# Optimization experiments

Hardware: AMD Instinct MI355X
Metric: run time of the kernel (lower is better)

## Reference

```python
import jax, jax.numpy as jnp
import numpy as np
from jax import lax

IN_CHANNELS = 64
PYRAMID_LEVELS = 3
SIGMA = 1.6
S_VALUE = 2.0 ** (1.0 / 3.0)


def _gaussian_kernel_2d(ksize, sigma):
    # matches cv2.getGaussianKernel: normalized 1D gaussian, then outer product
    ax = np.arange(ksize, dtype=np.float64) - (ksize - 1) / 2.0
    g = np.exp(-(ax ** 2) / (2.0 * sigma ** 2))
    g = g / g.sum()
    return np.outer(g, g).astype(np.float32)


def _depthwise_kernels():
    # list of (C, 1, k, k) depthwise kernels, k = 3, 5, 7
    ks = []
    for i in range(PYRAMID_LEVELS):
        k2d = _gaussian_kernel_2d(2 * i + 3, SIGMA * (S_VALUE ** i))
        w = np.broadcast_to(k2d[None, None], (IN_CHANNELS, 1) + k2d.shape)
        ks.append(jnp.asarray(np.ascontiguousarray(w)))
    return ks


def setup_inputs() -> dict:
    key = jax.random.key(0)
    x = jax.random.normal(key, (16, IN_CHANNELS, 256, 256), dtype=jnp.float32)
    return {"x": x}


def reference(x):
    B, C, H, W = x.shape
    kernels = _depthwise_kernels()
    G = x
    pyramid = [G]
    for w in kernels:
        G = lax.conv_general_dilated(
            G, w, window_strides=(1, 1), padding="SAME",
            feature_group_count=C,
            dimension_numbers=("NCHW", "OIHW", "NCHW"))
        pyramid.append(G)
    # Laplacian levels and their sum
    L0 = pyramid[0] - pyramid[1]
    L1 = pyramid[1] - pyramid[2]
    L2 = pyramid[2] - pyramid[3]
    context = (L0 + L1 + L2).reshape(B, C, H * W)  # (B, d, HW)
    att = jnp.einsum("bdn,ben->bde", jax.nn.softmax(context, axis=2), context)
    return att
```

## Files before the change

### kernel.cpp

```cpp
#include <hip/hip_runtime.h>
#include <hip/hip_bf16.h>
#include <math.h>

typedef short bf16x8 __attribute__((ext_vector_type(8)));
typedef float f32x4  __attribute__((ext_vector_type(4)));

struct WC   { float c[13]; };
struct G157 { float g3[3], g5[5], g7[7]; };

__device__ __forceinline__ unsigned short f2bf(float f) {
  __hip_bfloat16 h = __float2bfloat16(f);
  return *reinterpret_cast<unsigned short*>(&h);
}

__global__ __launch_bounds__(256) void zero_k(float* __restrict__ out, float* __restrict__ S,
                                              float* __restrict__ wtab, G157 gw) {
  int i = blockIdx.x * 256 + threadIdx.x;
  if (i < 65536) out[i] = 0.f;
  if (i < 1024) S[i] = 0.f;
  if (blockIdx.x == 0) {
    int g = threadIdx.x;
    float row[13];
    #pragma unroll
    for (int t = 0; t < 13; ++t) row[t] = 0.f;
    #pragma unroll
    for (int di = -3; di <= 3; ++di) {
      int ii = g + di;
      if ((unsigned)ii >= 256u) continue;
      float w7 = gw.g7[di + 3];
      #pragma unroll
      for (int dj = -2; dj <= 2; ++dj) {
        int jj = ii + dj;
        if ((unsigned)jj >= 256u) continue;
        float c2 = w7 * gw.g5[dj + 2];
        #pragma unroll
        for (int dk = -1; dk <= 1; ++dk) {
          int mm = jj + dk;
          if ((unsigned)mm >= 256u) continue;
          row[di + dj + dk + 6] += c2 * gw.g3[dk + 1];
        }
      }
    }
    #pragma unroll
    for (int t = 0; t < 13; ++t) wtab[(g << 4) + t] = row[t];
    wtab[(g << 4) + 13] = 0.f; wtab[(g << 4) + 14] = 0.f; wtab[(g << 4) + 15] = 0.f;
  }
}

__global__ __launch_bounds__(256) void ctx_k(const float* __restrict__ x,
                                             unsigned short* __restrict__ ctxb,
                                             const float* __restrict__ wtab,
                                             WC wc) {
  __shared__ __align__(16) float rb[2][8][272];
  __shared__ float vs[64][24];
  __shared__ float wl[96];

  const int tid = threadIdx.x;
  const int img = blockIdx.x >> 2;
  const int band = blockIdx.x & 3;
  const int y0 = band << 6;
  const float* xg = x + ((size_t)img << 16);
  unsigned short* cgb = ctxb + ((size_t)img << 16);

  if (tid < 96) wl[tid] = wtab[tid];
  {
    int bb = tid >> 7, rr = (tid >> 4) & 7, pp = tid & 15;
    rb[bb][rr][(pp < 8) ? pp : (256 + pp)] = 0.f;
  }

  float win[32];
  #pragma unroll
  for (int i = 0; i < 32; ++i) win[i] = 0.f;
  #pragma unroll
  for (int i = 0; i < 20; ++i) {
    int yy = y0 - 6 + i;
    if ((unsigned)yy < 256u) win[i] = xg[yy * 256 + tid];
  }
  __syncthreads();

  const bool vsave = (tid < 12) || (tid >= 244);
  const int vsidx = (tid < 12) ? tid : (tid - 232);
  const int g = tid >> 6, q = tid & 63;

  #pragma unroll
  for (int it = 0; it < 8; ++it) {
    const int y = y0 + 8 * it;
    #pragma unroll
    for (int j = 0; j < 8; ++j) {
      if (8 * it + 14 + j < 70) {
        int yy = y + 14 + j;
        float v = 0.f;
        if (yy < 256) v = xg[yy * 256 + tid];
        win[(8 * it + 20 + j) & 31] = v;
      }
    }
    float vv[8];
    const bool topb = (band == 0 && it == 0), botb = (band == 3 && it == 7);
    if (!topb && !botb) {
      #pragma unroll
      for (int r = 0; r < 8; ++r) {
        float a = 0.f;
        #pragma unroll
        for (int t = 0; t < 13; ++t) a += wc.c[t] * win[(8 * it + r + t) & 31];
        vv[r] = a;
      }
    } else {
      #pragma unroll
      for (int r = 0; r < 8; ++r) {
        int yr = y + r;
        float a = 0.f;
        if (yr < 6) {
          #pragma unroll
          for (int t = 0; t < 13; ++t) a += wl[(yr << 4) + t] * win[(8 * it + r + t) & 31];
        } else if (yr > 249) {
          #pragma unroll
          for (int t = 0; t < 13; ++t) a += wl[((255 - yr) << 4) + (12 - t)] * win[(8 * it + r + t) & 31];
        } else {
          #pragma unroll
          for (int t = 0; t < 13; ++t) a += wc.c[t] * win[(8 * it + r + t) & 31];
        }
        vv[r] = a;
      }
    }
    const int buf = it & 1;
    #pragma unroll
    for (int r = 0; r < 8; ++r) rb[buf][r][8 + tid] = vv[r];
    if (vsave) {
      #pragma unroll
      for (int r = 0; r < 8; ++r) vs[8 * it + r][vsidx] = vv[r];
    }
    __syncthreads();

    #pragma unroll
    for (int u = 0; u < 2; ++u) {
      const int rr = 2 * g + u;
      const int yy = y + rr;
      const float* hp = &rb[buf][rr][4 * q];
      float f[20];
      *(float4*)&f[0]  = *(const float4*)(hp + 0);
      *(float4*)&f[4]  = *(const float4*)(hp + 4);
      *(float4*)&f[8]  = *(const float4*)(hp + 8);
      *(float4*)&f[12] = *(const float4*)(hp + 12);
      *(float4*)&f[16] = *(const float4*)(hp + 16);
      float4 xq = *(const float4*)(xg + yy * 256 + 4 * q);
      float h0 = 0.f, h1 = 0.f, h2 = 0.f, h3 = 0.f;
      #pragma unroll
      for (int t = 0; t < 13; ++t) {
        float w = wc.c[t];
        h0 += w * f[2 + t]; h1 += w * f[3 + t]; h2 += w * f[4 + t]; h3 += w * f[5 + t];
      }
      unsigned short s0 = f2bf(xq.x - h0), s1 = f2bf(xq.y - h1);
      unsigned short s2 = f2bf(xq.z - h2), s3 = f2bf(xq.w - h3);
      *(ushort4*)(cgb + (size_t)yy * 256 + 4 * q) = make_ushort4(s0, s1, s2, s3);
    }
  }

  __syncthreads();
  #pragma unroll
  for (int k = 0; k < 3; ++k) {
    int e = k * 256 + tid;
    int row = e / 12;
    int ce = e - row * 12;
    int col = (ce < 6) ? ce : (244 + ce);
    float h = 0.f;
    if (ce < 6) {
      #pragma unroll
      for (int t = 0; t < 13; ++t) {
        int vc = col - 6 + t;
        if (vc >= 0) h += wl[(col << 4) + t] * vs[row][vc];
      }
    } else {
      #pragma unroll
      for (int t = 0; t < 13; ++t) {
        int vc = col - 6 + t;
        if (vc < 256) h += wl[((255 - col) << 4) + (12 - t)] * vs[row][vc - 232];
      }
    }
    int yrow = y0 + row;
    float xval = xg[yrow * 256 + col];
    cgb[yrow * 256 + col] = f2bf(xval - h);
  }
}

__global__ __launch_bounds__(256) void att_k(const unsigned short* __restrict__ ctxb,
                                             float* __restrict__ S,
                                             float* __restrict__ attacc) {
  const int t = threadIdx.x;
  const int wv = t >> 6, lane = t & 63;
  const int rw = lane & 15;
  const int kq = lane >> 4;
  const int ci = blockIdx.x;
  const int b = blockIdx.y;
  const unsigned short* cb = ctxb + ((size_t)b << 22);
  const int n0 = (ci << 10) + (kq << 3);

  const unsigned short* pA = cb + (((size_t)(16 * wv + rw)) << 16) + n0;
  const unsigned short* pB = cb + (((size_t)rw) << 16) + n0;

  f32x4 acc0 = {0.f, 0.f, 0.f, 0.f}, acc1 = acc0, acc2 = acc0, acc3 = acc0;
  float ssum = 0.f;

  #pragma unroll 8
  for (int ks = 0; ks < 1024; ks += 32) {
    bf16x8 av = *(const bf16x8*)(pA + ks);
    bf16x8 ev;
    const unsigned* au = (const unsigned*)&av;
    unsigned* eu = (unsigned*)&ev;
    #pragma unroll
    for (int j = 0; j < 4; ++j) {
      unsigned w = au[j];
      float elo = __expf(__uint_as_float(w << 16));
      float ehi = __expf(__uint_as_float(w & 0xffff0000u));
      ssum += elo + ehi;
      eu[j] = ((unsigned)f2bf(ehi) << 16) | (unsigned)f2bf(elo);
    }
    bf16x8 b0 = *(const bf16x8*)(pB + ks);
    bf16x8 b1 = *(const bf16x8*)(pB + (size_t)(16 << 16) + ks);
    bf16x8 b2 = *(const bf16x8*)(pB + (size_t)(32 << 16) + ks);
    bf16x8 b3 = *(const bf16x8*)(pB + (size_t)(48 << 16) + ks);
    acc0 = __builtin_amdgcn_mfma_f32_16x16x32_bf16(ev, b0, acc0, 0, 0, 0);
    acc1 = __builtin_amdgcn_mfma_f32_16x16x32_bf16(ev, b1, acc1, 0, 0, 0);
    acc2 = __builtin_amdgcn_mfma_f32_16x16x32_bf16(ev, b2, acc2, 0, 0, 0);
    acc3 = __builtin_amdgcn_mfma_f32_16x16x32_bf16(ev, b3, acc3, 0, 0, 0);
  }

  ssum += __shfl_xor(ssum, 16);
  ssum += __shfl_xor(ssum, 32);
  if (lane < 16) atomicAdd(&S[(b << 6) + (wv << 4) + rw], ssum);

  const int dl = kq << 2;
  float* ap = attacc + (((size_t)((b << 6) + (wv << 4) + dl)) << 6) + rw;
  #pragma unroll
  for (int reg = 0; reg < 4; ++reg) {
    atomicAdd(ap + ((size_t)reg << 6) + 0,  acc0[reg]);
    atomicAdd(ap + ((size_t)reg << 6) + 16, acc1[reg]);
    atomicAdd(ap + ((size_t)reg << 6) + 32, acc2[reg]);
    atomicAdd(ap + ((size_t)reg << 6) + 48, acc3[reg]);
  }
}

__global__ __launch_bounds__(256) void fin_k(float* __restrict__ out, const float* __restrict__ S) {
  int i = blockIdx.x * 256 + threadIdx.x;
  out[i] = out[i] / S[i >> 6];
}

extern "C" void kernel_launch(void* const* d_in, const int* in_sizes, int n_in,
                              void* d_out, int out_size, void* d_ws, size_t ws_size,
                              hipStream_t stream) {
  const float* x = (const float*)d_in[0];
  float* out = (float*)d_out;
  unsigned short* ctxb = (unsigned short*)d_ws;
  float* S    = (float*)((char*)d_ws + (size_t)67108864 * 2);
  float* wtab = (float*)((char*)d_ws + (size_t)67108864 * 2 + 4096);
  if (ws_size < (size_t)67108864 * 2 + 4096 + 16384) return;

  double gg[3][7];
  double sv = pow(2.0, 1.0 / 3.0);
  for (int lv = 0; lv < 3; ++lv) {
    int k = 2 * lv + 3;
    double sig = 1.6 * pow(sv, lv), sum = 0.0;
    for (int i = 0; i < k; ++i) {
      double a = i - (k - 1) / 2.0;
      gg[lv][i] = exp(-a * a / (2.0 * sig * sig));
      sum += gg[lv][i];
    }
    for (int i = 0; i < k; ++i) gg[lv][i] /= sum;
  }

  G157 gw;
  for (int i = 0; i < 3; ++i) gw.g3[i] = (float)gg[0][i];
  for (int i = 0; i < 5; ++i) gw.g5[i] = (float)gg[1][i];
  for (int i = 0; i < 7; ++i) gw.g7[i] = (float)gg[2][i];

  WC wc;
  {
    double t35[7] = {0};
    for (int i = 0; i < 3; ++i)
      for (int j = 0; j < 5; ++j) t35[i + j] += gg[0][i] * gg[1][j];
    double t357[13] = {0};
    for (int i = 0; i < 7; ++i)
      for (int j = 0; j < 7; ++j) t357[i + j] += t35[i] * gg[2][j];
    for (int t = 0; t < 13; ++t) wc.c[t] = (float)t357[t];
  }

  zero_k<<<dim3(256), dim3(256), 0, stream>>>(out, S, wtab, gw);
  ctx_k<<<dim3(4096), dim3(256), 0, stream>>>(x, ctxb, wtab, wc);
  att_k<<<dim3(64, 16), dim3(256), 0, stream>>>(ctxb, S, out);
  fin_k<<<dim3(256), dim3(256), 0, stream>>>(out, S);
}
```

Before: 207.8 us.

## Restructure context kernel into per-wave row strips without block barriers

The separable-blur context kernel now gives each wave its own 16-row strip. Each thread keeps a float4 register ring of input rows, and the horizontal pass goes through a wave-private shared buffer. This removes the per-iteration block-wide __syncthreads and the double-buffered row staging, and it reuses the centre input row from the ring instead of reloading it from global memory. Loads become vectorised float4, and launch bounds ask for three blocks per CU; the trade-off is more register pressure and reliance on in-order LDS access within a wave.

Result: slower. 218.3 us (+5.0%).

```diff
diff --git a/kernel.cpp b/kernel.cpp
--- a/kernel.cpp
+++ b/kernel.cpp
@@ -47,138 +47,140 @@
   }
 }
 
-__global__ __launch_bounds__(256) void ctx_k(const float* __restrict__ x,
-                                             unsigned short* __restrict__ ctxb,
-                                             const float* __restrict__ wtab,
-                                             WC wc) {
-  __shared__ __align__(16) float rb[2][8][272];
-  __shared__ float vs[64][24];
+__global__ __launch_bounds__(256, 3) void ctx_k(const float* __restrict__ x,
+                                                unsigned short* __restrict__ ctxb,
+                                                const float* __restrict__ wtab,
+                                                WC wc) {
+  __shared__ __align__(16) float vb[4][272];
+  __shared__ __align__(16) float evs[4][16][24];
   __shared__ float wl[96];
 
   const int tid = threadIdx.x;
-  const int img = blockIdx.x >> 2;
-  const int band = blockIdx.x & 3;
-  const int y0 = band << 6;
+  const int w = tid >> 6, q = tid & 63;
+  const int img = blockIdx.x >> 2, band = blockIdx.x & 3;
+  const int r0 = (band << 6) + (w << 4);
+  const int c0 = q << 2;
   const float* xg = x + ((size_t)img << 16);
   unsigned short* cgb = ctxb + ((size_t)img << 16);
 
   if (tid < 96) wl[tid] = wtab[tid];
-  {
-    int bb = tid >> 7, rr = (tid >> 4) & 7, pp = tid & 15;
-    rb[bb][rr][(pp < 8) ? pp : (256 + pp)] = 0.f;
-  }
-
-  float win[32];
-  #pragma unroll
-  for (int i = 0; i < 32; ++i) win[i] = 0.f;
-  #pragma unroll
-  for (int i = 0; i < 20; ++i) {
-    int yy = y0 - 6 + i;
-    if ((unsigned)yy < 256u) win[i] = xg[yy * 256 + tid];
+  if (q < 2) {
+    *(float4*)&vb[w][q << 2] = make_float4(0.f, 0.f, 0.f, 0.f);
+    *(float4*)&vb[w][264 + (q << 2)] = make_float4(0.f, 0.f, 0.f, 0.f);
   }
   __syncthreads();
 
-  const bool vsave = (tid < 12) || (tid >= 244);
-  const int vsidx = (tid < 12) ? tid : (tid - 232);
-  const int g = tid >> 6, q = tid & 63;
-
-  #pragma unroll
-  for (int it = 0; it < 8; ++it) {
-    const int y = y0 + 8 * it;
-    #pragma unroll
-    for (int j = 0; j < 8; ++j) {
-      if (8 * it + 14 + j < 70) {
-        int yy = y + 14 + j;
-        float v = 0.f;
-        if (yy < 256) v = xg[yy * 256 + tid];
-        win[(8 * it + 20 + j) & 31] = v;
-      }
-    }
-    float vv[8];
-    const bool topb = (band == 0 && it == 0), botb = (band == 3 && it == 7);
-    if (!topb && !botb) {
-      #pragma unroll
-      for (int r = 0; r < 8; ++r) {
-        float a = 0.f;
-        #pragma unroll
-        for (int t = 0; t < 13; ++t) a += wc.c[t] * win[(8 * it + r + t) & 31];
-        vv[r] = a;
+  float4 ring[16];
+  #pragma unroll
+  for (int i = 0; i < 15; ++i) {
+    int yy = r0 - 6 + i;
+    float4 v = make_float4(0.f, 0.f, 0.f, 0.f);
+    if ((unsigned)yy < 256u) v = *(const float4*)(xg + yy * 256 + c0);
+    ring[i] = v;
+  }
+  ring[15] = make_float4(0.f, 0.f, 0.f, 0.f);
+
+  #pragma unroll
+  for (int rr = 0; rr < 16; ++rr) {
+    {
+      int yy = r0 + rr + 9;
+      float4 v = make_float4(0.f, 0.f, 0.f, 0.f);
+      if (yy < 256) v = *(const float4*)(xg + yy * 256 + c0);
+      ring[(rr + 15) & 15] = v;
+    }
+    const int y = r0 + rr;
+
+    float ax = 0.f, ay = 0.f, az = 0.f, aw = 0.f;
+    if (rr >= 6 && rr <= 9) {
+      #pragma unroll
+      for (int t = 0; t < 13; ++t) {
+        float4 s = ring[(rr + t) & 15];
+        float wv = wc.c[t];
+        ax += wv * s.x; ay += wv * s.y; az += wv * s.z; aw += wv * s.w;
+      }
+    } else if (rr < 6) {
+      if (y >= 6) {
+        #pragma unroll
+        for (int t = 0; t < 13; ++t) {
+          float4 s = ring[(rr + t) & 15];
+          float wv = wc.c[t];
+          ax += wv * s.x; ay += wv * s.y; az += wv * s.z; aw += wv * s.w;
+        }
+      } else {
+        #pragma unroll
+        for (int t = 0; t < 13; ++t) {
+          float4 s = ring[(rr + t) & 15];
+          float wv = wl[(y << 4) + t];
+          ax += wv * s.x; ay += wv * s.y; az += wv * s.z; aw += wv * s.w;
+        }
       }
     } else {
-      #pragma unroll
-      for (int r = 0; r < 8; ++r) {
-        int yr = y + r;
-        float a = 0.f;
-        if (yr < 6) {
-          #pragma unroll
-          for (int t = 0; t < 13; ++t) a += wl[(yr << 4) + t] * win[(8 * it + r + t) & 31];
-        } else if (yr > 249) {
-          #pragma unroll
-          for (int t = 0; t < 13; ++t) a += wl[((255 - yr) << 4) + (12 - t)] * win[(8 * it + r + t) & 31];
-        } else {
-          #pragma unroll
-          for (int t = 0; t < 13; ++t) a += wc.c[t] * win[(8 * it + r + t) & 31];
-        }
-        vv[r] = a;
-      }
-    }
-    const int buf = it & 1;
-    #pragma unroll
-    for (int r = 0; r < 8; ++r) rb[buf][r][8 + tid] = vv[r];
-    if (vsave) {
-      #pragma unroll
-      for (int r = 0; r < 8; ++r) vs[8 * it + r][vsidx] = vv[r];
-    }
-    __syncthreads();
-
-    #pragma unroll
-    for (int u = 0; u < 2; ++u) {
-      const int rr = 2 * g + u;
-      const int yy = y + rr;
-      const float* hp = &rb[buf][rr][4 * q];
-      float f[20];
-      *(float4*)&f[0]  = *(const float4*)(hp + 0);
-      *(float4*)&f[4]  = *(const float4*)(hp + 4);
-      *(float4*)&f[8]  = *(const float4*)(hp + 8);
-      *(float4*)&f[12] = *(const float4*)(hp + 12);
-      *(float4*)&f[16] = *(const float4*)(hp + 16);
-      float4 xq = *(const float4*)(xg + yy * 256 + 4 * q);
-      float h0 = 0.f, h1 = 0.f, h2 = 0.f, h3 = 0.f;
-      #pragma unroll
-      for (int t = 0; t < 13; ++t) {
-        float w = wc.c[t];
-        h0 += w * f[2 + t]; h1 += w * f[3 + t]; h2 += w * f[4 + t]; h3 += w * f[5 + t];
-      }
-      unsigned short s0 = f2bf(xq.x - h0), s1 = f2bf(xq.y - h1);
-      unsigned short s2 = f2bf(xq.z - h2), s3 = f2bf(xq.w - h3);
-      *(ushort4*)(cgb + (size_t)yy * 256 + 4 * q) = make_ushort4(s0, s1, s2, s3);
-    }
-  }
-
-  __syncthreads();
+      if (y <= 249) {
+        #pragma unroll
+        for (int t = 0; t < 13; ++t) {
+          float4 s = ring[(rr + t) & 15];
+          float wv = wc.c[t];
+          ax += wv * s.x; ay += wv * s.y; az += wv * s.z; aw += wv * s.w;
+        }
+      } else {
+        #pragma unroll
+        for (int t = 0; t < 13; ++t) {
+          float4 s = ring[(rr + t) & 15];
+          float wv = wl[((255 - y) << 4) + (12 - t)];
+          ax += wv * s.x; ay += wv * s.y; az += wv * s.z; aw += wv * s.w;
+        }
+      }
+    }
+
+    float4 v4 = make_float4(ax, ay, az, aw);
+    *(float4*)&vb[w][8 + c0] = v4;
+    if (q < 3)       *(float4*)&evs[w][rr][c0] = v4;
+    else if (q >= 61) *(float4*)&evs[w][rr][12 + ((q - 61) << 2)] = v4;
+
+    const float* hp = &vb[w][c0];
+    float f[20];
+    *(float4*)&f[0]  = *(const float4*)(hp + 0);
+    *(float4*)&f[4]  = *(const float4*)(hp + 4);
+    *(float4*)&f[8]  = *(const float4*)(hp + 8);
+    *(float4*)&f[12] = *(const float4*)(hp + 12);
+    *(float4*)&f[16] = *(const float4*)(hp + 16);
+    float h0 = 0.f, h1 = 0.f, h2 = 0.f, h3 = 0.f;
+    #pragma unroll
+    for (int t = 0; t < 13; ++t) {
+      float wv = wc.c[t];
+      h0 += wv * f[2 + t]; h1 += wv * f[3 + t]; h2 += wv * f[4 + t]; h3 += wv * f[5 + t];
+    }
+    float4 xq = ring[(rr + 6) & 15];
+    unsigned short s0 = f2bf(xq.x - h0), s1 = f2bf(xq.y - h1);
+    unsigned short s2 = f2bf(xq.z - h2), s3 = f2bf(xq.w - h3);
+    *(ushort4*)(cgb + (size_t)y * 256 + c0) = make_ushort4(s0, s1, s2, s3);
+  }
+
   #pragma unroll
   for (int k = 0; k < 3; ++k) {
-    int e = k * 256 + tid;
+    int e = (k << 6) + q;
     int row = e / 12;
     int ce = e - row * 12;
+    int y = r0 + row;
     int col = (ce < 6) ? ce : (244 + ce);
     float h = 0.f;
     if (ce < 6) {
       #pragma unroll
       for (int t = 0; t < 13; ++t) {
         int vc = col - 6 + t;
-        if (vc >= 0) h += wl[(col << 4) + t] * vs[row][vc];
+        int vi = (vc < 0) ? 0 : vc;
+        h += wl[(col << 4) + t] * evs[w][row][vi];
       }
     } else {
       #pragma unroll
       for (int t = 0; t < 13; ++t) {
         int vc = col - 6 + t;
-        if (vc < 256) h += wl[((255 - col) << 4) + (12 - t)] * vs[row][vc - 232];
-      }
-    }
-    int yrow = y0 + row;
-    float xval = xg[yrow * 256 + col];
-    cgb[yrow * 256 + col] = f2bf(xval - h);
+        int vi = (vc > 255 ? 255 : vc) - 232;
+        h += wl[((255 - col) << 4) + (12 - t)] * evs[w][row][vi];
+      }
+    }
+    float xv = xg[(size_t)y * 256 + col];
+    cgb[(size_t)y * 256 + col] = f2bf(xv - h);
   }
 }
 
@@ -208,9 +210,9 @@
     unsigned* eu = (unsigned*)&ev;
     #pragma unroll
     for (int j = 0; j < 4; ++j) {
-      unsigned w = au[j];
-      float elo = __expf(__uint_as_float(w << 16));
-      float ehi = __expf(__uint_as_float(w & 0xffff0000u));
+      unsigned ww = au[j];
+      float elo = __expf(__uint_as_float(ww << 16));
+      float ehi = __expf(__uint_as_float(ww & 0xffff0000u));
       ssum += elo + ehi;
       eu[j] = ((unsigned)f2bf(ehi) << 16) | (unsigned)f2bf(elo);
     }
```
